# Kernel optimization log

Hardware: AMD Instinct MI355X
Metric: run time of the kernel (lower is better)

Reference implementation:

```python
import jax, jax.numpy as jnp
import numpy as np

N_NODES = 2_000_000
IN_CH = 64
OUT_CH = 128
NUM_GRAPHS = 16384


def setup_inputs() -> dict:
    key = jax.random.key(0)
    k1, k2, k3, k4 = jax.random.split(key, 4)
    x = jax.random.normal(k1, (N_NODES, IN_CH), dtype=jnp.float32)
    segment_ids = jnp.sort(
        jax.random.randint(k2, (N_NODES,), 0, NUM_GRAPHS, dtype=jnp.int64)
    )
    # nn.Linear(in, out): weight [out, in], bias [out]
    bound = 1.0 / np.sqrt(IN_CH)
    weight = jax.random.uniform(k3, (OUT_CH, IN_CH), dtype=jnp.float32,
                                minval=-bound, maxval=bound)
    bias = jax.random.uniform(k4, (OUT_CH,), dtype=jnp.float32,
                              minval=-bound, maxval=bound)
    return {"x": x, "segment_ids": segment_ids, "weight": weight,
            "bias": bias, "num_graphs": NUM_GRAPHS}


def reference(x, segment_ids, weight, bias, num_graphs):
    # Per-graph mean pooling (segment mean), then linear embed.
    sums = jax.ops.segment_sum(x, segment_ids, num_segments=num_graphs)  # [G, d]
    counts = jax.ops.segment_sum(jnp.ones((x.shape[0],), x.dtype),
                                 segment_ids, num_segments=num_graphs)  # [G]
    means = sums / counts[:, None]                                       # [G, d]
    return means @ weight.T + bias                                        # [G, out]
```

## Files before the change

kernel.cpp:

```cpp
#include <hip/hip_runtime.h>
#include <hip/hip_bf16.h>


#define IN_CH 64
#define OUT_CH 128
#define WPB 8
#define BLOCK (WPB * 64)

__global__ void seg_starts_kernel(const int* __restrict__ ids, int n, int G,
                                  int* __restrict__ starts) {
    int i = blockIdx.x * blockDim.x + threadIdx.x;
    if (i >= n) return;
    const int cur  = ids[i];
    const int prev = (i == 0) ? -1 : ids[i - 1];
    for (int g = prev + 1; g <= cur; ++g) starts[g] = i;
    if (i == n - 1) {
        for (int g = cur + 1; g <= G; ++g) starts[g] = n;
    }
}

__global__ __launch_bounds__(BLOCK) void pool_linear_kernel(
        const float* __restrict__ x, const float* __restrict__ W,
        const float* __restrict__ bias, const int* __restrict__ starts,
        float* __restrict__ out, int G) {
    __shared__ float w_lds[IN_CH * 129];

    const int t = threadIdx.x;
    for (int i = t; i < OUT_CH * IN_CH; i += BLOCK) {
        const int o = i >> 6;
        const int c = i & 63;
        w_lds[c * 129 + o] = W[i];
    }
    __syncthreads();

    const int wv = t >> 6;
    const int l  = t & 63;
    const int g  = blockIdx.x * WPB + wv;
    if (g >= G) return;

    const int rs = l >> 4;
    const int cq = (l & 15) << 2;

    const int s0 = starts[g];
    const int s1 = starts[g + 1];

    float4 a0 = make_float4(0.f, 0.f, 0.f, 0.f);
    float4 a1 = make_float4(0.f, 0.f, 0.f, 0.f);
    int r = s0;
    for (; r + 8 <= s1; r += 8) {
        const float4 v0 = *reinterpret_cast<const float4*>(x + (size_t)(r + rs)     * IN_CH + cq);
        const float4 v1 = *reinterpret_cast<const float4*>(x + (size_t)(r + 4 + rs) * IN_CH + cq);
        a0.x += v0.x; a0.y += v0.y; a0.z += v0.z; a0.w += v0.w;
        a1.x += v1.x; a1.y += v1.y; a1.z += v1.z; a1.w += v1.w;
    }
    if (r + 4 <= s1) {
        const float4 v = *reinterpret_cast<const float4*>(x + (size_t)(r + rs) * IN_CH + cq);
        a0.x += v.x; a0.y += v.y; a0.z += v.z; a0.w += v.w;
        r += 4;
    }
    if (r + rs < s1) {
        const float4 v = *reinterpret_cast<const float4*>(x + (size_t)(r + rs) * IN_CH + cq);
        a1.x += v.x; a1.y += v.y; a1.z += v.z; a1.w += v.w;
    }

    float sx = a0.x + a1.x;
    float sy = a0.y + a1.y;
    float sz = a0.z + a1.z;
    float sw = a0.w + a1.w;

    sx += __shfl_xor(sx, 16); sy += __shfl_xor(sy, 16);
    sz += __shfl_xor(sz, 16); sw += __shfl_xor(sw, 16);
    sx += __shfl_xor(sx, 32); sy += __shfl_xor(sy, 32);
    sz += __shfl_xor(sz, 32); sw += __shfl_xor(sw, 32);

    const float cnt = (float)(s1 - s0);
    const float m0 = sx / cnt;
    const float m1 = sy / cnt;
    const float m2 = sz / cnt;
    const float m3 = sw / cnt;

    float o0 = bias[l];
    float o1 = bias[l + 64];
    #pragma unroll
    for (int c = 0; c < IN_CH; ++c) {
        float m;
        switch (c & 3) {
            case 0:  m = __shfl(m0, c >> 2); break;
            case 1:  m = __shfl(m1, c >> 2); break;
            case 2:  m = __shfl(m2, c >> 2); break;
            default: m = __shfl(m3, c >> 2); break;
        }
        o0 = fmaf(w_lds[c * 129 + l],      m, o0);
        o1 = fmaf(w_lds[c * 129 + l + 64], m, o1);
    }
    out[(size_t)g * OUT_CH + l]      = o0;
    out[(size_t)g * OUT_CH + l + 64] = o1;
}

extern "C" void kernel_launch(void* const* d_in, const int* in_sizes, int n_in,
                              void* d_out, int out_size, void* d_ws, size_t ws_size,
                              hipStream_t stream) {
    const float* x    = (const float*)d_in[0];
    const int*   ids  = (const int*)d_in[1];
    const float* W    = (const float*)d_in[2];
    const float* bias = (const float*)d_in[3];
    float* out = (float*)d_out;

    const int N = in_sizes[1];
    const int G = out_size / OUT_CH;

    int* starts = (int*)d_ws;

    {
        const int block = 256;
        seg_starts_kernel<<<(N + block - 1) / block, block, 0, stream>>>(
            ids, N, G, starts);
    }
    {
        const int blocks = (G + WPB - 1) / WPB;
        pool_linear_kernel<<<blocks, BLOCK, 0, stream>>>(x, W, bias, starts, out, G);
    }
}
```

Baseline: 111.8 us.

## Fuse segment-start search into pooling kernel via binary search, use nontemporal loads

```diff
diff --git a/kernel.cpp b/kernel.cpp
--- a/kernel.cpp
+++ b/kernel.cpp
@@ -7,25 +7,37 @@
 #define WPB 8
 #define BLOCK (WPB * 64)
 
-__global__ void seg_starts_kernel(const int* __restrict__ ids, int n, int G,
-                                  int* __restrict__ starts) {
-    int i = blockIdx.x * blockDim.x + threadIdx.x;
-    if (i >= n) return;
-    const int cur  = ids[i];
-    const int prev = (i == 0) ? -1 : ids[i - 1];
-    for (int g = prev + 1; g <= cur; ++g) starts[g] = i;
-    if (i == n - 1) {
-        for (int g = cur + 1; g <= G; ++g) starts[g] = n;
-    }
-}
+typedef float f32x4 __attribute__((ext_vector_type(4)));
 
-__global__ __launch_bounds__(BLOCK) void pool_linear_kernel(
-        const float* __restrict__ x, const float* __restrict__ W,
-        const float* __restrict__ bias, const int* __restrict__ starts,
-        float* __restrict__ out, int G) {
+__global__ __launch_bounds__(BLOCK) void fused_pool_linear_kernel(
+        const float* __restrict__ x, const int* __restrict__ ids,
+        const float* __restrict__ W, const float* __restrict__ bias,
+        float* __restrict__ out, int N, int G) {
     __shared__ float w_lds[IN_CH * 129];
 
-    const int t = threadIdx.x;
+    const int t  = threadIdx.x;
+    const int wv = t >> 6;
+    const int l  = t & 63;
+    const int g  = blockIdx.x * WPB + wv;
+
+    int s0 = 0, s1 = 0;
+    if (g < G) {
+        const int target = g + (l & 1);
+        int lo = 0, hi = N;
+        const int guess = (int)(((long long)target * (long long)N) / (long long)G);
+        int wlo = guess - 4096; if (wlo < 0) wlo = 0;
+        int whi = guess + 4096; if (whi > N) whi = N;
+        const bool ok_lo = (wlo == 0) || (ids[wlo - 1] < target);
+        const bool ok_hi = (whi == N) || (ids[whi] >= target);
+        if (ok_lo && ok_hi) { lo = wlo; hi = whi; }
+        while (lo < hi) {
+            const int mid = (lo + hi) >> 1;
+            if (ids[mid] < target) lo = mid + 1; else hi = mid;
+        }
+        s0 = __shfl(lo, 0);
+        s1 = __shfl(lo, 1);
+    }
+
     for (int i = t; i < OUT_CH * IN_CH; i += BLOCK) {
         const int o = i >> 6;
         const int c = i & 63;
@@ -33,33 +45,31 @@
     }
     __syncthreads();
 
-    const int wv = t >> 6;
-    const int l  = t & 63;
-    const int g  = blockIdx.x * WPB + wv;
     if (g >= G) return;
 
     const int rs = l >> 4;
     const int cq = (l & 15) << 2;
 
-    const int s0 = starts[g];
-    const int s1 = starts[g + 1];
-
     float4 a0 = make_float4(0.f, 0.f, 0.f, 0.f);
     float4 a1 = make_float4(0.f, 0.f, 0.f, 0.f);
     int r = s0;
     for (; r + 8 <= s1; r += 8) {
-        const float4 v0 = *reinterpret_cast<const float4*>(x + (size_t)(r + rs)     * IN_CH + cq);
-        const float4 v1 = *reinterpret_cast<const float4*>(x + (size_t)(r + 4 + rs) * IN_CH + cq);
+        const f32x4 v0 = __builtin_nontemporal_load(
+            reinterpret_cast<const f32x4*>(x + (size_t)(r + rs) * IN_CH + cq));
+        const f32x4 v1 = __builtin_nontemporal_load(
+            reinterpret_cast<const f32x4*>(x + (size_t)(r + 4 + rs) * IN_CH + cq));
         a0.x += v0.x; a0.y += v0.y; a0.z += v0.z; a0.w += v0.w;
         a1.x += v1.x; a1.y += v1.y; a1.z += v1.z; a1.w += v1.w;
     }
     if (r + 4 <= s1) {
-        const float4 v = *reinterpret_cast<const float4*>(x + (size_t)(r + rs) * IN_CH + cq);
+        const f32x4 v = __builtin_nontemporal_load(
+            reinterpret_cast<const f32x4*>(x + (size_t)(r + rs) * IN_CH + cq));
         a0.x += v.x; a0.y += v.y; a0.z += v.z; a0.w += v.w;
         r += 4;
     }
     if (r + rs < s1) {
-        const float4 v = *reinterpret_cast<const float4*>(x + (size_t)(r + rs) * IN_CH + cq);
+        const f32x4 v = __builtin_nontemporal_load(
+            reinterpret_cast<const f32x4*>(x + (size_t)(r + rs) * IN_CH + cq));
         a1.x += v.x; a1.y += v.y; a1.z += v.z; a1.w += v.w;
     }
 
@@ -109,15 +119,7 @@
     const int N = in_sizes[1];
     const int G = out_size / OUT_CH;
 
-    int* starts = (int*)d_ws;
-
-    {
-        const int block = 256;
-        seg_starts_kernel<<<(N + block - 1) / block, block, 0, stream>>>(
-            ids, N, G, starts);
-    }
-    {
-        const int blocks = (G + WPB - 1) / WPB;
-        pool_linear_kernel<<<blocks, BLOCK, 0, stream>>>(x, W, bias, starts, out, G);
-    }
+    const int blocks = (G + WPB - 1) / WPB;
+    fused_pool_linear_kernel<<<blocks, BLOCK, 0, stream>>>(
+        x, ids, W, bias, out, N, G);
 }
```

New measurement: 100.6 us (median of 2 runs). 10.1% less time.
